# Optimization experiments

Hardware: AMD Instinct MI355X
Metric: run time of the kernel (lower is better)

Reference implementation:

```python
import jax, jax.numpy as jnp
import numpy as np

NEG_SLOPE = 0.2  # PyG GATConv default


def gat_conv(x, edge_index, W, a_src, a_dst, bias):
    """Single-head PyG-style GATConv (eval mode, add_self_loops=True)."""
    N = x.shape[0]
    h = x @ W  # [N, F_out]
    # add self loops
    loops = jnp.arange(N, dtype=edge_index.dtype)
    src = jnp.concatenate([edge_index[0], loops])  # [E+N]
    dst = jnp.concatenate([edge_index[1], loops])
    # per-edge attention logits: a_src . h_j + a_dst . h_i  (j=src, i=dst)
    alpha_s = h @ a_src  # [N]
    alpha_d = h @ a_dst  # [N]
    e = jax.nn.leaky_relu(alpha_s[src] + alpha_d[dst], NEG_SLOPE)  # [E+N]
    # segment softmax over incoming edges of each dst node
    m = jax.ops.segment_max(e, dst, num_segments=N)
    ex = jnp.exp(e - m[dst])
    denom = jax.ops.segment_sum(ex, dst, num_segments=N)
    alpha = ex / denom[dst]  # [E+N]
    # weighted scatter-aggregate of source features
    out = jax.ops.segment_sum(h[src] * alpha[:, None], dst, num_segments=N)
    return out + bias


def setup_inputs() -> dict:
    key = jax.random.key(0)
    ks = jax.random.split(key, 12)
    N, E = 100000, 3200000
    Fin, H, Fout = 128, 32, 32
    x = jax.random.normal(ks[0], (N, Fin), dtype=jnp.float32)
    edge_index = jax.random.randint(ks[1], (2, E), 0, N, dtype=jnp.int64)
    s = 1.0 / np.sqrt(Fin)
    W1 = jax.random.uniform(ks[2], (Fin, H), jnp.float32, -s, s)
    a1s = jax.random.uniform(ks[3], (H,), jnp.float32, -s, s)
    a1d = jax.random.uniform(ks[4], (H,), jnp.float32, -s, s)
    b1 = jnp.zeros((H,), jnp.float32)
    s2 = 1.0 / np.sqrt(H)
    W2 = jax.random.uniform(ks[5], (H, H), jnp.float32, -s2, s2)
    a2s = jax.random.uniform(ks[6], (H,), jnp.float32, -s2, s2)
    a2d = jax.random.uniform(ks[7], (H,), jnp.float32, -s2, s2)
    b2 = jnp.zeros((H,), jnp.float32)
    Wf = jax.random.uniform(ks[8], (H, Fout), jnp.float32, -s2, s2)
    bf = jax.random.uniform(ks[9], (Fout,), jnp.float32, -s2, s2)
    return {"x": x, "edge_index": edge_index, "W1": W1, "a1s": a1s, "a1d": a1d,
            "b1": b1, "W2": W2, "a2s": a2s, "a2d": a2d, "b2": b2,
            "Wf": Wf, "bf": bf}


def reference(x, edge_index, W1, a1s, a1d, b1, W2, a2s, a2d, b2, Wf, bf):
    h = jax.nn.relu(gat_conv(x, edge_index, W1, a1s, a1d, b1))
    h = jax.nn.relu(gat_conv(h, edge_index, W2, a2s, a2d, b2))
    return h @ Wf + bf
```

## Files before the change

kernel.cpp:

```cpp
#include <hip/hip_runtime.h>

#define NEG_SLOPE 0.2f
#define BK_LOG 9
#define BK_NODES (1 << BK_LOG)
#define TILE_EPT 24
#define TILE_E (256 * TILE_EPT)

typedef __attribute__((ext_vector_type(8))) short bf8_t;
typedef __attribute__((ext_vector_type(4))) float f32x4;

__device__ __forceinline__ float leaky(float v) { return v > 0.0f ? v : NEG_SLOPE * v; }

__device__ __forceinline__ unsigned short f2bf(float f) {
    unsigned u = __float_as_uint(f);
    u += 0x7fffu + ((u >> 16) & 1u);
    return (unsigned short)(u >> 16);
}
__device__ __forceinline__ float bf2f(unsigned short h) {
    return __uint_as_float(((unsigned)h) << 16);
}

__device__ __forceinline__ int scan256_excl(int v, int* tmp) {
    int t = threadIdx.x;
    tmp[t] = v;
    __syncthreads();
    for (int d = 1; d < 256; d <<= 1) {
        int x = (t >= d) ? tmp[t - d] : 0;
        __syncthreads();
        tmp[t] += x;
        __syncthreads();
    }
    int r = tmp[t] - v;
    __syncthreads();
    return r;
}

__device__ __forceinline__ void wsplit_body(int blk, int tid,
                                            const float* __restrict__ W,
                                            unsigned short* __restrict__ wh,
                                            unsigned short* __restrict__ wl, int K) {
    int idx = blk * 256 + tid;
    int KT = K >> 5;
    if (idx >= KT * 128) return;
    int lane = idx & 63;
    int nt = (idx >> 6) & 1;
    int kt = idx >> 7;
    int q = lane >> 4, c = lane & 15;
#pragma unroll
    for (int j = 0; j < 8; ++j) {
        int k = kt * 32 + q * 8 + j;
        int n = nt * 16 + c;
        float w = W[k * 32 + n];
        unsigned short hi = f2bf(w);
        wh[idx * 8 + j] = hi;
        wl[idx * 8 + j] = f2bf(w - bf2f(hi));
    }
}

__global__ __launch_bounds__(256) void k_prep(
    const float* __restrict__ W1, unsigned short* __restrict__ wh1, unsigned short* __restrict__ wl1,
    const float* __restrict__ W2, unsigned short* __restrict__ wh2, unsigned short* __restrict__ wl2,
    const float* __restrict__ Wf, unsigned short* __restrict__ whf, unsigned short* __restrict__ wlf,
    int* __restrict__ bcnt)
{
    int b = blockIdx.x, t = threadIdx.x;
    if (b < 2)       wsplit_body(b, t, W1, wh1, wl1, 128);
    else if (b == 2) wsplit_body(0, t, W2, wh2, wl2, 32);
    else if (b == 3) wsplit_body(0, t, Wf, whf, wlf, 32);
    else             bcnt[t] = 0;
}

template <int FIN, bool ATT>
__device__ __forceinline__ void gemm_body(
    int blk, int tid,
    const float* __restrict__ x,
    const unsigned short* __restrict__ wh, const unsigned short* __restrict__ wl,
    const float* __restrict__ a_s, const float* __restrict__ a_d,
    const float* __restrict__ bias,
    float* __restrict__ h, float* __restrict__ alpha_s,
    float* __restrict__ alpha_d, int N)
{
    constexpr int KT = FIN / 32;
    int lane = tid & 63;
    int mt   = blk * 4 + (tid >> 6);
    int m0   = mt * 16;
    if (m0 >= N) return;
    int q = lane >> 4, c = lane & 15;

    bf8_t Bh[KT][2], Bl[KT][2];
#pragma unroll
    for (int kt = 0; kt < KT; ++kt)
#pragma unroll
        for (int nt = 0; nt < 2; ++nt) {
            Bh[kt][nt] = *(const bf8_t*)(wh + ((size_t)(kt * 2 + nt) * 64 + lane) * 8);
            Bl[kt][nt] = *(const bf8_t*)(wl + ((size_t)(kt * 2 + nt) * 64 + lane) * 8);
        }

    int rowa = m0 + c;
    if (rowa >= N) rowa = N - 1;
    const float* xr = x + (size_t)rowa * FIN;
    bf8_t Ah[KT], Al[KT];
#pragma unroll
    for (int kt = 0; kt < KT; ++kt) {
        f32x4 v0 = *(const f32x4*)(xr + kt * 32 + q * 8);
        f32x4 v1 = *(const f32x4*)(xr + kt * 32 + q * 8 + 4);
#pragma unroll
        for (int j = 0; j < 8; ++j) {
            float f = (j < 4) ? v0[j] : v1[j - 4];
            unsigned short hi = f2bf(f);
            Ah[kt][j] = (short)hi;
            Al[kt][j] = (short)f2bf(f - bf2f(hi));
        }
    }

    f32x4 acc0 = {0.f, 0.f, 0.f, 0.f}, acc1 = {0.f, 0.f, 0.f, 0.f};
#pragma unroll
    for (int kt = 0; kt < KT; ++kt) {
        acc0 = __builtin_amdgcn_mfma_f32_16x16x32_bf16(Ah[kt], Bh[kt][0], acc0, 0, 0, 0);
        acc1 = __builtin_amdgcn_mfma_f32_16x16x32_bf16(Ah[kt], Bh[kt][1], acc1, 0, 0, 0);
        acc0 = __builtin_amdgcn_mfma_f32_16x16x32_bf16(Al[kt], Bh[kt][0], acc0, 0, 0, 0);
        acc1 = __builtin_amdgcn_mfma_f32_16x16x32_bf16(Al[kt], Bh[kt][1], acc1, 0, 0, 0);
        acc0 = __builtin_amdgcn_mfma_f32_16x16x32_bf16(Ah[kt], Bl[kt][0], acc0, 0, 0, 0);
        acc1 = __builtin_amdgcn_mfma_f32_16x16x32_bf16(Ah[kt], Bl[kt][1], acc1, 0, 0, 0);
    }

#pragma unroll
    for (int reg = 0; reg < 4; ++reg) {
        int r = m0 + q * 4 + reg;
        if (r < N) {
            float v0s = acc0[reg], v1s = acc1[reg];
            if (!ATT) { v0s += bias[c]; v1s += bias[c + 16]; }
            h[(size_t)r * 32 + c]      = v0s;
            h[(size_t)r * 32 + 16 + c] = v1s;
        }
    }
    if (ATT) {
        float as0 = a_s[c], as1 = a_s[c + 16];
        float ad0 = a_d[c], ad1 = a_d[c + 16];
#pragma unroll
        for (int reg = 0; reg < 4; ++reg) {
            float ps = acc0[reg] * as0 + acc1[reg] * as1;
            float pd = acc0[reg] * ad0 + acc1[reg] * ad1;
#pragma unroll
            for (int msk = 8; msk >= 1; msk >>= 1) {
                ps += __shfl_xor(ps, msk);
                pd += __shfl_xor(pd, msk);
            }
            int r = m0 + q * 4 + reg;
            if (c == 0 && r < N) {
                alpha_s[r] = ps;
                alpha_d[r] = pd;
            }
        }
    }
}

template <int FIN, bool ATT>
__global__ __launch_bounds__(256) void gemm_mfma(
    const float* __restrict__ x,
    const unsigned short* __restrict__ wh, const unsigned short* __restrict__ wl,
    const float* __restrict__ a_s, const float* __restrict__ a_d,
    const float* __restrict__ bias,
    float* __restrict__ h, float* __restrict__ alpha_s,
    float* __restrict__ alpha_d, int N)
{
    gemm_body<FIN, ATT>(blockIdx.x, threadIdx.x, x, wh, wl, a_s, a_d, bias,
                        h, alpha_s, alpha_d, N);
}

__global__ __launch_bounds__(256) void k_bcount_gemm1(
    const int* __restrict__ edst, int* __restrict__ bcnt, int E, int nb_tile,
    const float* __restrict__ x,
    const unsigned short* __restrict__ wh, const unsigned short* __restrict__ wl,
    const float* __restrict__ a_s, const float* __restrict__ a_d,
    float* __restrict__ h, float* __restrict__ alpha_s,
    float* __restrict__ alpha_d, int N)
{
    if ((int)blockIdx.x < nb_tile) {
        __shared__ int th[256];
        int t = threadIdx.x;
        th[t] = 0;
        __syncthreads();
        int base = blockIdx.x * TILE_E;
#pragma unroll
        for (int k = 0; k < TILE_EPT; ++k) {
            int e = base + t + k * 256;
            if (e < E) atomicAdd(&th[edst[e] >> BK_LOG], 1);
        }
        __syncthreads();
        if (th[t]) atomicAdd(&bcnt[t], th[t]);
    } else {
        gemm_body<128, true>(blockIdx.x - nb_tile, threadIdx.x, x, wh, wl,
                             a_s, a_d, nullptr, h, alpha_s, alpha_d, N);
    }
}


__global__ __launch_bounds__(256) void k_bscan(const int* __restrict__ bcnt,
                                               int* __restrict__ bbase,
                                               int* __restrict__ bcur,
                                               int* __restrict__ off, int N, int E) {
    __shared__ int tmp[256];
    int t = threadIdx.x;
    int ex = scan256_excl(bcnt[t], tmp);
    bbase[t] = ex;
    bcur[t]  = ex;
    if (t == 0) { bbase[256] = E; off[N] = E; }
}

__global__ __launch_bounds__(256) void k_bplace(const int* __restrict__ esrc,
                                                const int* __restrict__ edst,
                                                int* __restrict__ bcur,
                                                unsigned* __restrict__ pairs, int E) {
    __shared__ int2 sp[TILE_E];
    __shared__ int th[256], tx[256], rb[256], tmp[256];
    int t = threadIdx.x;
    th[t] = 0;
    __syncthreads();
    int base = blockIdx.x * TILE_E;
    int tot  = min(TILE_E, E - base);
#pragma unroll
    for (int k = 0; k < TILE_EPT; ++k) {
        int e = base + t + k * 256;
        if (e < E) atomicAdd(&th[edst[e] >> BK_LOG], 1);
    }
    __syncthreads();
    int cnt = th[t];
    tx[t] = scan256_excl(cnt, tmp);
    rb[t] = atomicAdd(&bcur[t], cnt);
    th[t] = 0;
    __syncthreads();
#pragma unroll
    for (int k = 0; k < TILE_EPT; ++k) {
        int e = base + t + k * 256;
        if (e < E) {
            int s = esrc[e], d = edst[e];
            int b = d >> BK_LOG;
            int r = atomicAdd(&th[b], 1);
            sp[tx[b] + r] = make_int2(s, d);
        }
    }
    __syncthreads();
    for (int i = t; i < tot; i += 256) {
        int2 p = sp[i];
        int  b = p.y >> BK_LOG;
        pairs[rb[b] + (i - tx[b])] =
            ((unsigned)p.x << BK_LOG) | (unsigned)(p.y & (BK_NODES - 1));
    }
}

__global__ __launch_bounds__(512) void k_csr(const int* __restrict__ bbase,
                                             const unsigned* __restrict__ pairs,
                                             int* __restrict__ off,
                                             int* __restrict__ csr, int N) {
    __shared__ int lh[BK_NODES], lx[BK_NODES];
    int b = blockIdx.x, t = threadIdx.x;
    int lo = bbase[b], hi = bbase[b + 1];
    int node0 = b << BK_LOG;
    lh[t] = 0;
    __syncthreads();
    for (int j = lo + t; j < hi; j += 512)
        atomicAdd(&lh[pairs[j] & (BK_NODES - 1)], 1);
    __syncthreads();
    lx[t] = lh[t];
    __syncthreads();
    for (int d = 1; d < BK_NODES; d <<= 1) {
        int x0 = (t >= d) ? lx[t - d] : 0;
        __syncthreads();
        lx[t] += x0;
        __syncthreads();
    }
    lx[t] -= lh[t];
    if (node0 + t < N) off[node0 + t] = lo + lx[t];
    lh[t] = 0;
    __syncthreads();
    for (int j = lo + t; j < hi; j += 512) {
        unsigned p  = pairs[j];
        int      li = p & (BK_NODES - 1);
        int      r  = atomicAdd(&lh[li], 1);
        csr[lo + lx[li] + r] = (int)(p >> BK_LOG);
    }
}

__global__ __launch_bounds__(256) void fused_agg(
    const int* __restrict__ csr, const int* __restrict__ off,
    const float* __restrict__ alpha_s, const float* __restrict__ alpha_d,
    const float* __restrict__ h, const float* __restrict__ bias,
    float* __restrict__ out, int N)
{
    int t = blockIdx.x * 256 + threadIdx.x;
    int i = t >> 3, q = t & 7;
    if (i >= N) return;
    int s0 = off[i], s1 = off[i + 1];
    float ad = alpha_d[i];

    const float* hq = h + q * 4;

    float w   = __expf(leaky(alpha_s[i] + ad));
    float den = w;
    f32x4 hv  = *(const f32x4*)(hq + (size_t)i * 32);
    f32x4 acc;
    acc[0] = w * hv[0]; acc[1] = w * hv[1]; acc[2] = w * hv[2]; acc[3] = w * hv[3];

    for (int j = s0; j < s1; j += 32) {
        int i0 = j + q, i1 = i0 + 8, i2 = i0 + 16, i3 = i0 + 24;
        int c0 = (i0 < s1) ? csr[i0] : 0;
        int c1 = (i1 < s1) ? csr[i1] : 0;
        int c2 = (i2 < s1) ? csr[i2] : 0;
        int c3 = (i3 < s1) ? csr[i3] : 0;
        float e0x = __expf(leaky(alpha_s[c0] + ad));
        float e1x = __expf(leaky(alpha_s[c1] + ad));
        float e2x = __expf(leaky(alpha_s[c2] + ad));
        float e3x = __expf(leaky(alpha_s[c3] + ad));
        float w0 = (i0 < s1) ? e0x : 0.0f;
        float w1 = (i1 < s1) ? e1x : 0.0f;
        float w2 = (i2 < s1) ? e2x : 0.0f;
        float w3 = (i3 < s1) ? e3x : 0.0f;
        int o0 = c0 << 5, o1 = c1 << 5, o2 = c2 << 5, o3 = c3 << 5;
#pragma unroll
        for (int e = 0; e < 8; ++e) {
            int   e0 = __shfl(o0, e, 8); float f0 = __shfl(w0, e, 8);
            int   e1 = __shfl(o1, e, 8); float f1 = __shfl(w1, e, 8);
            int   e2 = __shfl(o2, e, 8); float f2 = __shfl(w2, e, 8);
            int   e3 = __shfl(o3, e, 8); float f3 = __shfl(w3, e, 8);
            f32x4 g0 = *(const f32x4*)(hq + e0);
            f32x4 g1 = *(const f32x4*)(hq + e1);
            f32x4 g2 = *(const f32x4*)(hq + e2);
            f32x4 g3 = *(const f32x4*)(hq + e3);
            den += (f0 + f1) + (f2 + f3);
            acc[0] += f0 * g0[0]; acc[1] += f0 * g0[1];
            acc[2] += f0 * g0[2]; acc[3] += f0 * g0[3];
            acc[0] += f1 * g1[0]; acc[1] += f1 * g1[1];
            acc[2] += f1 * g1[2]; acc[3] += f1 * g1[3];
            acc[0] += f2 * g2[0]; acc[1] += f2 * g2[1];
            acc[2] += f2 * g2[2]; acc[3] += f2 * g2[3];
            acc[0] += f3 * g3[0]; acc[1] += f3 * g3[1];
            acc[2] += f3 * g3[2]; acc[3] += f3 * g3[3];
        }
    }

    float inv = 1.0f / den;
    f32x4 b4  = *(const f32x4*)(bias + q * 4);
    f32x4 r;
    r[0] = fmaxf(acc[0] * inv + b4[0], 0.0f);
    r[1] = fmaxf(acc[1] * inv + b4[1], 0.0f);
    r[2] = fmaxf(acc[2] * inv + b4[2], 0.0f);
    r[3] = fmaxf(acc[3] * inv + b4[3], 0.0f);
    *(f32x4*)(out + (size_t)i * 32 + q * 4) = r;
}

extern "C" void kernel_launch(void* const* d_in, const int* in_sizes, int n_in,
                              void* d_out, int out_size, void* d_ws, size_t ws_size,
                              hipStream_t stream)
{
    const float* x   = (const float*)d_in[0];
    const int*   ei  = (const int*)d_in[1];
    const float* W1  = (const float*)d_in[2];
    const float* a1s = (const float*)d_in[3];
    const float* a1d = (const float*)d_in[4];
    const float* b1  = (const float*)d_in[5];
    const float* W2  = (const float*)d_in[6];
    const float* a2s = (const float*)d_in[7];
    const float* a2d = (const float*)d_in[8];
    const float* b2  = (const float*)d_in[9];
    const float* Wf  = (const float*)d_in[10];
    const float* bf  = (const float*)d_in[11];

    const int N = in_sizes[0] / 128;
    const int E = in_sizes[1] / 2;
    const int* esrc = ei;
    const int* edst = ei + E;
    const int B1 = (N + BK_NODES - 1) >> BK_LOG;

    float* ws = (float*)d_ws;
    float* h1      = ws;
    float* h2      = h1 + (size_t)N * 32;
    float* alpha_s = h2 + (size_t)N * 32;
    float* alpha_d = alpha_s + N;
    int*   off     = (int*)(alpha_d + N);
    int*   csr     = off + (N + 1);
    int*   bcnt    = csr + E;
    int*   bbase   = bcnt + 256;
    int*   bcur    = bbase + 257;
    unsigned short* wfb =
        (unsigned short*)(((uintptr_t)(bcur + 256) + 15) & ~(uintptr_t)15);
    unsigned short* wh1 = wfb;
    unsigned short* wl1 = wh1 + 4096;
    unsigned short* wh2 = wl1 + 4096;
    unsigned short* wl2 = wh2 + 1024;
    unsigned short* whf = wl2 + 1024;
    unsigned short* wlf = whf + 1024;
    unsigned* pairs = ((size_t)E <= (size_t)32 * N)
                          ? (unsigned*)h2
                          : (unsigned*)(wlf + 1024);

    const int nb_agg  = (N * 8 + 255) / 256;
    const int nb_tile = (E + TILE_E - 1) / TILE_E;
    const int nb_gemm = ((N + 15) / 16 + 3) / 4;

    k_prep<<<5, 256, 0, stream>>>(W1, wh1, wl1, W2, wh2, wl2, Wf, whf, wlf, bcnt);

    k_bcount_gemm1<<<nb_tile + nb_gemm, 256, 0, stream>>>(
        edst, bcnt, E, nb_tile, x, wh1, wl1, a1s, a1d, h1, alpha_s, alpha_d, N);

    k_bscan  <<<1, 256, 0, stream>>>(bcnt, bbase, bcur, off, N, E);
    k_bplace <<<nb_tile, 256, 0, stream>>>(esrc, edst, bcur, pairs, E);
    k_csr    <<<B1, 512, 0, stream>>>(bbase, pairs, off, csr, N);

    fused_agg<<<nb_agg, 256, 0, stream>>>(csr, off, alpha_s, alpha_d, h1, b1, h2, N);

    gemm_mfma<32, true><<<nb_gemm, 256, 0, stream>>>(
        h2, wh2, wl2, a2s, a2d, nullptr, h1, alpha_s, alpha_d, N);
    fused_agg<<<nb_agg, 256, 0, stream>>>(csr, off, alpha_s, alpha_d, h1, b2, h2, N);

    gemm_mfma<32, false><<<nb_gemm, 256, 0, stream>>>(
        h2, whf, wlf, nullptr, nullptr, bf, (float*)d_out, nullptr, nullptr, N);
}
```

Baseline: 339.0 us.

## Fuse 32x32 layer GEMMs into aggregation epilogue and prefetch next edge chunk

Each fused_agg now multiplies its aggregated output by the next layer's 32x32 weight in registers. The non-final pass also computes the next layer's attention logits, and the final pass adds the output bias. This removes the two separate MFMA GEMM launches, their h round-trips, and the bf16 hi/lo weight splits for W2 and Wf. The aggregation loop also prefetches the next chunk's csr indices and alpha_s values to overlap gather latency. In exchange, the epilogue adds per-thread FP32 FMAs, shuffles and weight reads, plus extra alpha buffers so the aggregation does not overwrite its own inputs.

```diff
diff --git a/kernel.cpp b/kernel.cpp
--- a/kernel.cpp
+++ b/kernel.cpp
@@ -59,24 +59,19 @@
 
 __global__ __launch_bounds__(256) void k_prep(
     const float* __restrict__ W1, unsigned short* __restrict__ wh1, unsigned short* __restrict__ wl1,
-    const float* __restrict__ W2, unsigned short* __restrict__ wh2, unsigned short* __restrict__ wl2,
-    const float* __restrict__ Wf, unsigned short* __restrict__ whf, unsigned short* __restrict__ wlf,
     int* __restrict__ bcnt)
 {
     int b = blockIdx.x, t = threadIdx.x;
-    if (b < 2)       wsplit_body(b, t, W1, wh1, wl1, 128);
-    else if (b == 2) wsplit_body(0, t, W2, wh2, wl2, 32);
-    else if (b == 3) wsplit_body(0, t, Wf, whf, wlf, 32);
-    else             bcnt[t] = 0;
-}
-
-template <int FIN, bool ATT>
+    if (b < 2) wsplit_body(b, t, W1, wh1, wl1, 128);
+    else       bcnt[t] = 0;
+}
+
+template <int FIN>
 __device__ __forceinline__ void gemm_body(
     int blk, int tid,
     const float* __restrict__ x,
     const unsigned short* __restrict__ wh, const unsigned short* __restrict__ wl,
     const float* __restrict__ a_s, const float* __restrict__ a_d,
-    const float* __restrict__ bias,
     float* __restrict__ h, float* __restrict__ alpha_s,
     float* __restrict__ alpha_d, int N)
 {
@@ -128,44 +123,27 @@
     for (int reg = 0; reg < 4; ++reg) {
         int r = m0 + q * 4 + reg;
         if (r < N) {
-            float v0s = acc0[reg], v1s = acc1[reg];
-            if (!ATT) { v0s += bias[c]; v1s += bias[c + 16]; }
-            h[(size_t)r * 32 + c]      = v0s;
-            h[(size_t)r * 32 + 16 + c] = v1s;
-        }
-    }
-    if (ATT) {
-        float as0 = a_s[c], as1 = a_s[c + 16];
-        float ad0 = a_d[c], ad1 = a_d[c + 16];
-#pragma unroll
-        for (int reg = 0; reg < 4; ++reg) {
-            float ps = acc0[reg] * as0 + acc1[reg] * as1;
-            float pd = acc0[reg] * ad0 + acc1[reg] * ad1;
-#pragma unroll
-            for (int msk = 8; msk >= 1; msk >>= 1) {
-                ps += __shfl_xor(ps, msk);
-                pd += __shfl_xor(pd, msk);
-            }
-            int r = m0 + q * 4 + reg;
-            if (c == 0 && r < N) {
-                alpha_s[r] = ps;
-                alpha_d[r] = pd;
-            }
-        }
-    }
-}
-
-template <int FIN, bool ATT>
-__global__ __launch_bounds__(256) void gemm_mfma(
-    const float* __restrict__ x,
-    const unsigned short* __restrict__ wh, const unsigned short* __restrict__ wl,
-    const float* __restrict__ a_s, const float* __restrict__ a_d,
-    const float* __restrict__ bias,
-    float* __restrict__ h, float* __restrict__ alpha_s,
-    float* __restrict__ alpha_d, int N)
-{
-    gemm_body<FIN, ATT>(blockIdx.x, threadIdx.x, x, wh, wl, a_s, a_d, bias,
-                        h, alpha_s, alpha_d, N);
+            h[(size_t)r * 32 + c]      = acc0[reg];
+            h[(size_t)r * 32 + 16 + c] = acc1[reg];
+        }
+    }
+    float as0 = a_s[c], as1 = a_s[c + 16];
+    float ad0 = a_d[c], ad1 = a_d[c + 16];
+#pragma unroll
+    for (int reg = 0; reg < 4; ++reg) {
+        float ps = acc0[reg] * as0 + acc1[reg] * as1;
+        float pd = acc0[reg] * ad0 + acc1[reg] * ad1;
+#pragma unroll
+        for (int msk = 8; msk >= 1; msk >>= 1) {
+            ps += __shfl_xor(ps, msk);
+            pd += __shfl_xor(pd, msk);
+        }
+        int r = m0 + q * 4 + reg;
+        if (c == 0 && r < N) {
+            alpha_s[r] = ps;
+            alpha_d[r] = pd;
+        }
+    }
 }
 
 __global__ __launch_bounds__(256) void k_bcount_gemm1(
@@ -190,8 +168,8 @@
         __syncthreads();
         if (th[t]) atomicAdd(&bcnt[t], th[t]);
     } else {
-        gemm_body<128, true>(blockIdx.x - nb_tile, threadIdx.x, x, wh, wl,
-                             a_s, a_d, nullptr, h, alpha_s, alpha_d, N);
+        gemm_body<128>(blockIdx.x - nb_tile, threadIdx.x, x, wh, wl,
+                       a_s, a_d, h, alpha_s, alpha_d, N);
     }
 }
 
@@ -282,11 +260,16 @@
     }
 }
 
+template <bool FINAL>
 __global__ __launch_bounds__(256) void fused_agg(
     const int* __restrict__ csr, const int* __restrict__ off,
     const float* __restrict__ alpha_s, const float* __restrict__ alpha_d,
     const float* __restrict__ h, const float* __restrict__ bias,
-    float* __restrict__ out, int N)
+    const float* __restrict__ Wn,
+    const float* __restrict__ an_s, const float* __restrict__ an_d,
+    const float* __restrict__ bn,
+    float* __restrict__ outh,
+    float* __restrict__ out_as, float* __restrict__ out_ad, int N)
 {
     int t = blockIdx.x * 256 + threadIdx.x;
     int i = t >> 3, q = t & 7;
@@ -302,20 +285,33 @@
     f32x4 acc;
     acc[0] = w * hv[0]; acc[1] = w * hv[1]; acc[2] = w * hv[2]; acc[3] = w * hv[3];
 
+    int   c0 = 0, c1 = 0, c2 = 0, c3 = 0;
+    float a0 = 0.f, a1 = 0.f, a2 = 0.f, a3 = 0.f;
+    {
+        int i0 = s0 + q;
+        c0 = (i0      < s1) ? csr[i0]      : 0;
+        c1 = (i0 + 8  < s1) ? csr[i0 + 8]  : 0;
+        c2 = (i0 + 16 < s1) ? csr[i0 + 16] : 0;
+        c3 = (i0 + 24 < s1) ? csr[i0 + 24] : 0;
+        a0 = alpha_s[c0]; a1 = alpha_s[c1]; a2 = alpha_s[c2]; a3 = alpha_s[c3];
+    }
     for (int j = s0; j < s1; j += 32) {
-        int i0 = j + q, i1 = i0 + 8, i2 = i0 + 16, i3 = i0 + 24;
-        int c0 = (i0 < s1) ? csr[i0] : 0;
-        int c1 = (i1 < s1) ? csr[i1] : 0;
-        int c2 = (i2 < s1) ? csr[i2] : 0;
-        int c3 = (i3 < s1) ? csr[i3] : 0;
-        float e0x = __expf(leaky(alpha_s[c0] + ad));
-        float e1x = __expf(leaky(alpha_s[c1] + ad));
-        float e2x = __expf(leaky(alpha_s[c2] + ad));
-        float e3x = __expf(leaky(alpha_s[c3] + ad));
-        float w0 = (i0 < s1) ? e0x : 0.0f;
-        float w1 = (i1 < s1) ? e1x : 0.0f;
-        float w2 = (i2 < s1) ? e2x : 0.0f;
-        float w3 = (i3 < s1) ? e3x : 0.0f;
+        int jn = j + 32;
+        int n0 = 0, n1 = 0, n2 = 0, n3 = 0;
+        if (jn < s1) {
+            int i0 = jn + q;
+            n0 = (i0      < s1) ? csr[i0]      : 0;
+            n1 = (i0 + 8  < s1) ? csr[i0 + 8]  : 0;
+            n2 = (i0 + 16 < s1) ? csr[i0 + 16] : 0;
+            n3 = (i0 + 24 < s1) ? csr[i0 + 24] : 0;
+        }
+        int i0 = j + q;
+        float w0 = (i0      < s1) ? __expf(leaky(a0 + ad)) : 0.0f;
+        float w1 = (i0 + 8  < s1) ? __expf(leaky(a1 + ad)) : 0.0f;
+        float w2 = (i0 + 16 < s1) ? __expf(leaky(a2 + ad)) : 0.0f;
+        float w3 = (i0 + 24 < s1) ? __expf(leaky(a3 + ad)) : 0.0f;
+        float na0 = alpha_s[n0], na1 = alpha_s[n1];
+        float na2 = alpha_s[n2], na3 = alpha_s[n3];
         int o0 = c0 << 5, o1 = c1 << 5, o2 = c2 << 5, o3 = c3 << 5;
 #pragma unroll
         for (int e = 0; e < 8; ++e) {
@@ -337,6 +333,8 @@
             acc[0] += f3 * g3[0]; acc[1] += f3 * g3[1];
             acc[2] += f3 * g3[2]; acc[3] += f3 * g3[3];
         }
+        c0 = n0; c1 = n1; c2 = n2; c3 = n3;
+        a0 = na0; a1 = na1; a2 = na2; a3 = na3;
     }
 
     float inv = 1.0f / den;
@@ -346,7 +344,40 @@
     r[1] = fmaxf(acc[1] * inv + b4[1], 0.0f);
     r[2] = fmaxf(acc[2] * inv + b4[2], 0.0f);
     r[3] = fmaxf(acc[3] * inv + b4[3], 0.0f);
-    *(f32x4*)(out + (size_t)i * 32 + q * 4) = r;
+
+    f32x4 m = {0.f, 0.f, 0.f, 0.f};
+#pragma unroll
+    for (int e = 0; e < 8; ++e) {
+        f32x4 rv;
+        rv[0] = __shfl(r[0], e, 8);
+        rv[1] = __shfl(r[1], e, 8);
+        rv[2] = __shfl(r[2], e, 8);
+        rv[3] = __shfl(r[3], e, 8);
+#pragma unroll
+        for (int jj = 0; jj < 4; ++jj) {
+            f32x4 wr = *(const f32x4*)(Wn + (e * 4 + jj) * 32 + q * 4);
+            m[0] += rv[jj] * wr[0]; m[1] += rv[jj] * wr[1];
+            m[2] += rv[jj] * wr[2]; m[3] += rv[jj] * wr[3];
+        }
+    }
+
+    if (FINAL) {
+        f32x4 bb = *(const f32x4*)(bn + q * 4);
+        m[0] += bb[0]; m[1] += bb[1]; m[2] += bb[2]; m[3] += bb[3];
+        *(f32x4*)(outh + (size_t)i * 32 + q * 4) = m;
+    } else {
+        *(f32x4*)(outh + (size_t)i * 32 + q * 4) = m;
+        f32x4 as4 = *(const f32x4*)(an_s + q * 4);
+        f32x4 ad4 = *(const f32x4*)(an_d + q * 4);
+        float ps = m[0] * as4[0] + m[1] * as4[1] + m[2] * as4[2] + m[3] * as4[3];
+        float pd = m[0] * ad4[0] + m[1] * ad4[1] + m[2] * ad4[2] + m[3] * ad4[3];
+#pragma unroll
+        for (int msk = 4; msk >= 1; msk >>= 1) {
+            ps += __shfl_xor(ps, msk, 8);
+            pd += __shfl_xor(pd, msk, 8);
+        }
+        if (q == 0) { out_as[i] = ps; out_ad[i] = pd; }
+    }
 }
 
 extern "C" void kernel_launch(void* const* d_in, const int* in_sizes, int n_in,
@@ -373,32 +404,30 @@
     const int B1 = (N + BK_NODES - 1) >> BK_LOG;
 
     float* ws = (float*)d_ws;
-    float* h1      = ws;
-    float* h2      = h1 + (size_t)N * 32;
-    float* alpha_s = h2 + (size_t)N * 32;
-    float* alpha_d = alpha_s + N;
-    int*   off     = (int*)(alpha_d + N);
-    int*   csr     = off + (N + 1);
-    int*   bcnt    = csr + E;
-    int*   bbase   = bcnt + 256;
-    int*   bcur    = bbase + 257;
+    float* h1       = ws;
+    float* h2       = h1 + (size_t)N * 32;
+    float* alpha_s  = h2 + (size_t)N * 32;
+    float* alpha_d  = alpha_s + N;
+    float* alpha_s2 = alpha_d + N;
+    float* alpha_d2 = alpha_s2 + N;
+    int*   off      = (int*)(alpha_d2 + N);
+    int*   csr      = off + (N + 1);
+    int*   bcnt     = csr + E;
+    int*   bbase    = bcnt + 256;
+    int*   bcur     = bbase + 257;
     unsigned short* wfb =
         (unsigned short*)(((uintptr_t)(bcur + 256) + 15) & ~(uintptr_t)15);
     unsigned short* wh1 = wfb;
     unsigned short* wl1 = wh1 + 4096;
-    unsigned short* wh2 = wl1 + 4096;
-    unsigned short* wl2 = wh2 + 1024;
-    unsigned short* whf = wl2 + 1024;
-    unsigned short* wlf = whf + 1024;
     unsigned* pairs = ((size_t)E <= (size_t)32 * N)
                           ? (unsigned*)h2
-                          : (unsigned*)(wlf + 1024);
+                          : (unsigned*)(wl1 + 4096);
 
     const int nb_agg  = (N * 8 + 255) / 256;
     const int nb_tile = (E + TILE_E - 1) / TILE_E;
     const int nb_gemm = ((N + 15) / 16 + 3) / 4;
 
-    k_prep<<<5, 256, 0, stream>>>(W1, wh1, wl1, W2, wh2, wl2, Wf, whf, wlf, bcnt);
+    k_prep<<<3, 256, 0, stream>>>(W1, wh1, wl1, bcnt);
 
     k_bcount_gemm1<<<nb_tile + nb_gemm, 256, 0, stream>>>(
         edst, bcnt, E, nb_tile, x, wh1, wl1, a1s, a1d, h1, alpha_s, alpha_d, N);
@@ -407,12 +436,11 @@
     k_bplace <<<nb_tile, 256, 0, stream>>>(esrc, edst, bcur, pairs, E);
     k_csr    <<<B1, 512, 0, stream>>>(bbase, pairs, off, csr, N);
 
-    fused_agg<<<nb_agg, 256, 0, stream>>>(csr, off, alpha_s, alpha_d, h1, b1, h2, N);
-
-    gemm_mfma<32, true><<<nb_gemm, 256, 0, stream>>>(
-        h2, wh2, wl2, a2s, a2d, nullptr, h1, alpha_s, alpha_d, N);
-    fused_agg<<<nb_agg, 256, 0, stream>>>(csr, off, alpha_s, alpha_d, h1, b2, h2, N);
-
-    gemm_mfma<32, false><<<nb_gemm, 256, 0, stream>>>(
-        h2, whf, wlf, nullptr, nullptr, bf, (float*)d_out, nullptr, nullptr, N);
-}
+    fused_agg<false><<<nb_agg, 256, 0, stream>>>(
+        csr, off, alpha_s, alpha_d, h1, b1, W2, a2s, a2d, nullptr,
+        h2, alpha_s2, alpha_d2, N);
+
+    fused_agg<true><<<nb_agg, 256, 0, stream>>>(
+        csr, off, alpha_s2, alpha_d2, h2, b2, Wf, nullptr, nullptr, bf,
+        (float*)d_out, nullptr, nullptr, N);
+}
```

Measured after the change: 338.4 us. No clear change (-0.2%).
